# Performance work log

Hardware: AMD Instinct MI355X
Metric: run time of the kernel (lower is better)

Reference implementation:

```python
import jax, jax.numpy as jnp
import numpy as np

B, N, C = 2, 784, 384
D_STATE, D_CONV, EXPAND = 64, 4, 2
D_INNER = EXPAND * C           # 768
DT_RANK = -(-C // 16)          # 24
NB, BS = 4, C // 4             # EinFFT blocks
SCALE = 0.02


def setup_inputs() -> dict:
    key = jax.random.key(0)
    ks = jax.random.split(key, 16)
    rn = lambda k, s, sc=SCALE: jax.random.normal(k, s, jnp.float32) * sc
    A = jnp.tile(jnp.arange(1, D_STATE + 1, dtype=jnp.float32), (D_INNER, 1))
    return {
        'x': jax.random.normal(ks[0], (B, N, C), jnp.float32),
        'H': 28, 'W': 28,
        'ln1_w': jnp.ones((C,), jnp.float32), 'ln1_b': jnp.zeros((C,), jnp.float32),
        'in_proj_w': rn(ks[1], (2 * D_INNER, C)),
        'conv_w': rn(ks[2], (D_INNER, 1, D_CONV), 0.1),
        'conv_b': jnp.zeros((D_INNER,), jnp.float32),
        'x_proj_w': rn(ks[3], (DT_RANK + 2 * D_STATE, D_INNER)),
        'dt_proj_w': rn(ks[4], (D_INNER, DT_RANK), 0.1),
        'dt_proj_b': rn(ks[5], (D_INNER,), 0.1),
        'A_log': jnp.log(A),
        'Dp': jnp.ones((D_INNER,), jnp.float32),
        'out_proj_w': rn(ks[6], (C, D_INNER)),
        'ln2_w': jnp.ones((C,), jnp.float32), 'ln2_b': jnp.zeros((C,), jnp.float32),
        'cw1': rn(ks[7], (2, NB, BS, BS)), 'cb1': rn(ks[8], (2, NB, BS)),
        'cw2': rn(ks[9], (2, NB, BS, BS)), 'cb2': rn(ks[10], (2, NB, BS)),
    }


def _ln(x, w, b, eps=1e-5):
    mu = x.mean(-1, keepdims=True)
    var = ((x - mu) ** 2).mean(-1, keepdims=True)
    return (x - mu) * jax.lax.rsqrt(var + eps) * w + b


def _silu(x):
    return x * jax.nn.sigmoid(x)


def _mamba(x, in_proj_w, conv_w, conv_b, x_proj_w, dt_proj_w, dt_proj_b, A_log, Dp, out_proj_w):
    Bb, L, _ = x.shape
    di, ds = A_log.shape
    dt_rank = dt_proj_w.shape[1]
    xz = x @ in_proj_w.T                       # [B,L,2*di]
    xi, z = jnp.split(xz, 2, axis=-1)
    # causal depthwise conv1d (pad left d_conv-1)
    xc = jax.lax.conv_general_dilated(
        xi.transpose(0, 2, 1), conv_w, (1,), [(conv_w.shape[-1] - 1, 0)],
        feature_group_count=di, dimension_numbers=('NCH', 'OIH', 'NCH'))
    xc = _silu(xc + conv_b[None, :, None]).transpose(0, 2, 1)  # [B,L,di]
    dbl = xc @ x_proj_w.T
    dt, Bs, Cs = jnp.split(dbl, [dt_rank, dt_rank + ds], axis=-1)
    dt = jax.nn.softplus(dt @ dt_proj_w.T + dt_proj_b)          # [B,L,di]
    A = -jnp.exp(A_log)                                          # [di,ds]

    def step(h, inp):
        dt_t, B_t, C_t, u_t = inp                                # [B,di],[B,ds],[B,ds],[B,di]
        dA = jnp.exp(dt_t[:, :, None] * A)                       # [B,di,ds]
        h = h * dA + dt_t[:, :, None] * B_t[:, None, :] * u_t[:, :, None]
        y = jnp.einsum('bds,bs->bd', h, C_t)
        return h, y

    h0 = jnp.zeros((Bb, di, ds), x.dtype)
    xs = (dt.transpose(1, 0, 2), Bs.transpose(1, 0, 2), Cs.transpose(1, 0, 2), xc.transpose(1, 0, 2))
    _, ys = jax.lax.scan(step, h0, xs)                           # [L,B,di]
    y = ys.transpose(1, 0, 2) + xc * Dp
    y = y * _silu(z)
    return y @ out_proj_w.T


def _einfft(x, cw1, cb1, cw2, cb2, lam=0.01):
    Bb, Nn, Cc = x.shape
    nb, bs = cw1.shape[1], cw1.shape[2]
    xf = jnp.fft.fft2(x.reshape(Bb, Nn, nb, bs), axes=(1, 2), norm='ortho')
    mul = lambda t, w: jnp.einsum('...bd,bdk->...bk', t, w)
    r1 = jax.nn.relu(mul(xf.real, cw1[0]) - mul(xf.imag, cw1[1]) + cb1[0])
    i1 = jax.nn.relu(mul(xf.real, cw1[1]) + mul(xf.imag, cw1[0]) + cb1[1])
    r2 = mul(r1, cw2[0]) - mul(i1, cw2[1]) + cb2[0]
    i2 = mul(r1, cw2[1]) + mul(i1, cw2[0]) + cb2[1]
    shrink = lambda v: jnp.sign(v) * jnp.maximum(jnp.abs(v) - lam, 0.0)
    xcplx = shrink(r2) + 1j * shrink(i2)
    out = jnp.fft.ifft2(xcplx, axes=(1, 2), norm='ortho').real.astype(jnp.float32)
    return out.reshape(Bb, Nn, Cc)


def reference(x, H, W, ln1_w, ln1_b, in_proj_w, conv_w, conv_b, x_proj_w,
              dt_proj_w, dt_proj_b, A_log, Dp, out_proj_w, ln2_w, ln2_b,
              cw1, cb1, cw2, cb2):
    x = x + _mamba(_ln(x, ln1_w, ln1_b), in_proj_w, conv_w, conv_b, x_proj_w,
                   dt_proj_w, dt_proj_b, A_log, Dp, out_proj_w)
    x = x + _einfft(_ln(x, ln2_w, ln2_b), cw1, cb1, cw2, cb2)
    return x
```

## Files before the change

kernel.cpp:

```cpp
#include <hip/hip_runtime.h>
#include <math.h>

#define BB 2
#define NN 784
#define CC 384
#define DI 768
#define DS 64
#define DTR 24
#define ROWS (BB*NN)
#define NC 16
#define LC 49

typedef __attribute__((ext_vector_type(8))) short bf16x8;
typedef __attribute__((ext_vector_type(4))) float f32x4;

static __device__ inline short f2bf(float f){
  unsigned u = __float_as_uint(f);
  unsigned r = (u + 0x7fffu + ((u>>16)&1u)) >> 16;
  return (short)r;
}
static __device__ inline float bf2f(short v){
  return __uint_as_float(((unsigned)(unsigned short)v)<<16);
}
static __device__ inline float rdlane(float v, int t){
  return __uint_as_float(__builtin_amdgcn_readlane(__float_as_uint(v), t));
}
template<int CTRL>
static __device__ inline float qp_add(float x){
  int t = __builtin_amdgcn_update_dpp(0, __float_as_int(x), CTRL, 0xf, 0xf, false);
  return x + __int_as_float(t);
}
#define QP_XOR1 0xB1
#define QP_XOR2 0x4E
#define LOG2E 1.44269504088896f

__global__ void k_zero4(float4* __restrict__ p, int n4){
  int i = blockIdx.x*256 + threadIdx.x;
  if (i < n4) p[i] = make_float4(0.f,0.f,0.f,0.f);
}

__global__ void k_ln(const float* __restrict__ x, const float* __restrict__ w,
                     const float* __restrict__ b, short* __restrict__ out, int rows){
  int row = blockIdx.x;
  if (row >= rows) return;
  int lane = threadIdx.x;
  const float* xr = x + (size_t)row*CC;
  float v[6]; float s = 0.f;
#pragma unroll
  for (int i=0;i<6;i++){ v[i] = xr[lane + 64*i]; s += v[i]; }
#pragma unroll
  for (int o=32;o;o>>=1) s += __shfl_xor(s,o);
  float mu = s * (1.f/CC);
  float vs = 0.f;
#pragma unroll
  for (int i=0;i<6;i++){ float d=v[i]-mu; vs += d*d; }
#pragma unroll
  for (int o=32;o;o>>=1) vs += __shfl_xor(vs,o);
  float rstd = rsqrtf(vs*(1.f/CC) + 1e-5f);
  short* orow = out + (size_t)row*CC;
#pragma unroll
  for (int i=0;i<6;i++){ int c = lane+64*i; orow[c] = f2bf((v[i]-mu)*rstd*w[c] + b[c]); }
}

__global__ void k_lnT(const float* __restrict__ x, const float* __restrict__ w,
                      const float* __restrict__ b, short* __restrict__ out){
  int row = blockIdx.x;
  if (row >= ROWS) return;
  int bb = row / NN, n = row % NN;
  int lane = threadIdx.x;
  const float* xr = x + (size_t)row*CC;
  float v[6]; float s = 0.f;
#pragma unroll
  for (int i=0;i<6;i++){ v[i] = xr[lane + 64*i]; s += v[i]; }
#pragma unroll
  for (int o=32;o;o>>=1) s += __shfl_xor(s,o);
  float mu = s * (1.f/CC);
  float vs = 0.f;
#pragma unroll
  for (int i=0;i<6;i++){ float d=v[i]-mu; vs += d*d; }
#pragma unroll
  for (int o=32;o;o>>=1) vs += __shfl_xor(vs,o);
  float rstd = rsqrtf(vs*(1.f/CC) + 1e-5f);
  short* ob = out + (size_t)bb*301056 + n;
#pragma unroll
  for (int i=0;i<6;i++){ int c = lane+64*i; ob[(size_t)c*NN] = f2bf((v[i]-mu)*rstd*w[c] + b[c]); }
}

template<int EPI, int ABF, int BBF, int SPLITK>
__global__ __launch_bounds__(256) void k_mgemm(
    const void* __restrict__ Ap, int lda, long long Azs,
    const void* __restrict__ Bp, int ldb, long long Bzs,
    const float* __restrict__ aux, int ldaux, long long auxzs,
    float* __restrict__ Y, int ldo, long long Ozs,
    int M, int N, int K, float alpha)
{
  __shared__ __align__(16) short As[64*32];
  __shared__ __align__(16) short Bs[64*32];
  int bz = blockIdx.z;
  int z  = bz / SPLITK, ks = bz % SPLITK;
  if (EPI == 1 || EPI == 2 || EPI == 3) aux += (size_t)z*auxzs;
  Y += (size_t)z*Ozs;
  int nk = (K + 31) >> 5;
  int per = (nk + SPLITK - 1) / SPLITK;
  int kbeg = ks*per*32;
  int kend = kbeg + per*32; if (kend > K) kend = K;
  if (kend <= kbeg) return;
  int ntile = (kend - kbeg + 31) >> 5;
  int m0 = blockIdx.y*64, n0 = blockIdx.x*64;
  int t = threadIdx.x;
  int srow = t>>2, skg = t&3;
  int w = t>>6, lane = t&63;
  int wr = (w>>1)*32, wc = (w&1)*32;
  int l15 = lane&15, lh = lane>>4;
  f32x4 acc[2][2] = {};
  int sslot = skg ^ ((srow>>1)&3);
  int gmA = m0 + srow, gnB = n0 + srow;
  int gko = skg*8;

  bf16x8 vA = {}, vB = {};
  float4 fA0, fA1, fB0, fB1;

  auto LOAD = [&](int k0){
    int gk = k0 + gko;
    if (ABF){
      bf16x8 v = {};
      if (gmA < M && gk < K) v = *(const bf16x8*)((const short*)Ap + (size_t)z*Azs + (size_t)gmA*lda + gk);
      vA = v;
    } else {
      fA0 = make_float4(0.f,0.f,0.f,0.f); fA1 = fA0;
      if (gmA < M && gk < K){
        const float* p = (const float*)Ap + (size_t)z*Azs + (size_t)gmA*lda + gk;
        fA0 = *(const float4*)p; fA1 = *(const float4*)(p+4);
      }
    }
    if (BBF){
      bf16x8 v = {};
      if (gnB < N && gk < K) v = *(const bf16x8*)((const short*)Bp + (size_t)z*Bzs + (size_t)gnB*ldb + gk);
      vB = v;
    } else {
      fB0 = make_float4(0.f,0.f,0.f,0.f); fB1 = fB0;
      if (gnB < N && gk < K){
        const float* p = (const float*)Bp + (size_t)z*Bzs + (size_t)gnB*ldb + gk;
        fB0 = *(const float4*)p; fB1 = *(const float4*)(p+4);
      }
    }
  };
  auto STORE = [&](){
    if (ABF) *(bf16x8*)(As + srow*32 + sslot*8) = vA;
    else {
      union { short s[8]; bf16x8 v; } pk;
      pk.s[0]=f2bf(fA0.x); pk.s[1]=f2bf(fA0.y); pk.s[2]=f2bf(fA0.z); pk.s[3]=f2bf(fA0.w);
      pk.s[4]=f2bf(fA1.x); pk.s[5]=f2bf(fA1.y); pk.s[6]=f2bf(fA1.z); pk.s[7]=f2bf(fA1.w);
      *(bf16x8*)(As + srow*32 + sslot*8) = pk.v;
    }
    if (BBF) *(bf16x8*)(Bs + srow*32 + sslot*8) = vB;
    else {
      union { short s[8]; bf16x8 v; } pk;
      pk.s[0]=f2bf(fB0.x); pk.s[1]=f2bf(fB0.y); pk.s[2]=f2bf(fB0.z); pk.s[3]=f2bf(fB0.w);
      pk.s[4]=f2bf(fB1.x); pk.s[5]=f2bf(fB1.y); pk.s[6]=f2bf(fB1.z); pk.s[7]=f2bf(fB1.w);
      *(bf16x8*)(Bs + srow*32 + sslot*8) = pk.v;
    }
  };

  LOAD(kbeg);
  for (int ti=0; ti<ntile; ++ti){
    STORE();
    __syncthreads();
    if (ti+1 < ntile) LOAD(kbeg + (ti+1)*32);
    bf16x8 af[2], bfr[2];
#pragma unroll
    for (int mi=0; mi<2; mi++){
      int row = wr + mi*16 + l15;
      af[mi] = *(const bf16x8*)(As + row*32 + ((lh ^ ((row>>1)&3))<<3));
    }
#pragma unroll
    for (int ni=0; ni<2; ni++){
      int col = wc + ni*16 + l15;
      bfr[ni] = *(const bf16x8*)(Bs + col*32 + ((lh ^ ((col>>1)&3))<<3));
    }
#pragma unroll
    for (int mi=0; mi<2; mi++)
#pragma unroll
      for (int ni=0; ni<2; ni++)
        acc[mi][ni] = __builtin_amdgcn_mfma_f32_16x16x32_bf16(af[mi], bfr[ni], acc[mi][ni], 0, 0, 0);
    __syncthreads();
  }
#pragma unroll
  for (int mi=0; mi<2; mi++){
#pragma unroll
    for (int ni=0; ni<2; ni++){
      int col = n0 + wc + ni*16 + l15;
      if (col >= N) continue;
#pragma unroll
      for (int j=0; j<4; j++){
        int row = m0 + wr + mi*16 + lh*4 + j;
        if (row >= M) continue;
        float v = acc[mi][ni][j];
        if (EPI == 0){ Y[(size_t)row*ldo + col] = v*alpha; }
        else if (EPI == 1){ Y[(size_t)row*ldo + col] = v*alpha + aux[(size_t)row*ldaux + col]; }
        else if (EPI == 2){ v += aux[col]; Y[(size_t)row*ldo + col] = fmaxf(v, 0.f); }
        else if (EPI == 3){ v += aux[col]; Y[(size_t)row*ldo + col] = copysignf(fmaxf(fabsf(v)-0.01f, 0.f), v); }
        else { atomicAdd(&Y[(size_t)row*ldo + col], v*alpha); }
      }
    }
  }
}

#define GBM 64
#define GBN 64
#define GBK 16
__global__ __launch_bounds__(256) void k_gemm(
    const float* __restrict__ X, int lda,
    const float* __restrict__ W,
    const float* __restrict__ bias,
    float* __restrict__ Y,
    int M, int N, int K)
{
  __shared__ float As[GBK][GBM+4];
  __shared__ float Bs[GBK][GBN+4];
  int m0 = blockIdx.y*GBM, n0 = blockIdx.x*GBN;
  int tid = threadIdx.x;
  int ty = tid>>4, tx = tid&15;
  float acc[4][4] = {{0.f}};
  for (int k0=0;k0<K;k0+=GBK){
#pragma unroll
    for (int l=0;l<4;l++){
      int e = tid + 256*l;
      int m = e>>4, kk = e&15;
      int gm = m0+m, gk = k0+kk;
      As[kk][m] = (gm<M && gk<K) ? X[(size_t)gm*lda+gk] : 0.f;
      int gn = n0+m;
      Bs[kk][m] = (gn<N && gk<K) ? W[(size_t)gn*K+gk] : 0.f;
    }
    __syncthreads();
#pragma unroll
    for (int kk=0;kk<GBK;kk++){
      float4 av = *(const float4*)&As[kk][ty*4];
      float4 bv = *(const float4*)&Bs[kk][tx*4];
      float a[4]={av.x,av.y,av.z,av.w}, b[4]={bv.x,bv.y,bv.z,bv.w};
#pragma unroll
      for (int i=0;i<4;i++)
#pragma unroll
        for (int j=0;j<4;j++) acc[i][j] += a[i]*b[j];
    }
    __syncthreads();
  }
#pragma unroll
  for (int i=0;i<4;i++){
    int gm = m0+ty*4+i; if (gm>=M) continue;
#pragma unroll
    for (int j=0;j<4;j++){
      int gn = n0+tx*4+j; if (gn>=N) continue;
      float v = acc[i][j] + bias[gn];
      v = (v>20.f)? v : log1pf(expf(v));
      Y[(size_t)gm*N+gn] = v;
    }
  }
}

__global__ void k_conv(const float* __restrict__ xz, const float* __restrict__ cw,
                       const float* __restrict__ cb, float* __restrict__ xc){
  int idx = blockIdx.x*256 + threadIdx.x;
  if (idx >= ROWS*DI) return;
  int d = idx % DI;
  int r = idx / DI;
  int b = r / NN, l = r % NN;
  float acc = cb[d];
#pragma unroll
  for (int t=0;t<4;t++){
    int ls = l-3+t;
    if (ls>=0) acc += cw[d*4+t] * xz[((size_t)(b*NN+ls))*1536 + d];
  }
  xc[(size_t)r*DI + d] = acc / (1.f + expf(-acc));
}

__global__ __launch_bounds__(256) void k_scan1(
    const float* __restrict__ dbl, const float* __restrict__ dtb,
    const float* __restrict__ xc, const float* __restrict__ A_log,
    short* __restrict__ hpart, float* __restrict__ sdt)
{
  __shared__ float Sb[LC*64];
  int gx = blockIdx.x;
  int bc = gx & 31, dgrp = gx >> 5;
  int b = bc >> 4, c = bc & 15;
  int wv = threadIdx.x >> 6, lane = threadIdx.x & 63;
  int d = dgrp*4 + wv;
  int t0 = c*LC;
  const float* dbr = dbl + ((size_t)(b*NN+t0))*152 + DTR;
  for (int i = threadIdx.x; i < LC*64; i += 256){
    int r = i >> 6, col = i & 63;
    Sb[i] = dbr[(size_t)r*152 + col];
  }
  __syncthreads();
  float A2 = -__expf(A_log[d*DS + lane]) * LOG2E;
  const float* dtp = dtb + ((size_t)(b*NN+t0))*DI + d;
  const float* up  = xc  + ((size_t)(b*NN+t0))*DI + d;
  float dt0v = (lane<LC) ? dtp[(size_t)lane*DI] : 0.f;
  float u0v  = (lane<LC) ? up[(size_t)lane*DI]  : 0.f;
  float du0v = dt0v * u0v;
  float h = 0.f;
  for (int tb=0; tb<LC; tb+=7){
    float e[7], f[7];
#pragma unroll
    for (int j=0;j<7;j++){
      int t = tb+j;
      float dt = rdlane(dt0v, t);
      float du = rdlane(du0v, t);
      e[j] = exp2f(dt*A2);
      f[j] = du*Sb[t*64 + lane];
    }
#pragma unroll
    for (int j=0;j<7;j++) h = h*e[j] + f[j];
  }
  int bd = b*DI + d;
  hpart[((size_t)bd*NC + c)*DS + lane] = f2bf(h);
  float s = dt0v;
#pragma unroll
  for (int o=32;o;o>>=1) s += __shfl_xor(s,o);
  if (lane==0) sdt[bd*NC + c] = s;
}

__global__ __launch_bounds__(256) void k_scan2(
    const float* __restrict__ sdt, const float* __restrict__ A_log,
    short* __restrict__ hpart)
{
  int wid = (blockIdx.x*256 + threadIdx.x) >> 6;
  int lane = threadIdx.x & 63;
  if (wid >= BB*DI) return;
  int d = wid % DI;
  float A = -__expf(A_log[d*DS + lane]);
  short* hp = hpart + (size_t)wid*NC*DS + lane;
  const float* sp = sdt + wid*NC;
  float part[NC], pA[NC];
#pragma unroll
  for (int c=0;c<NC;c++){ part[c] = bf2f(hp[(size_t)c*DS]); pA[c] = __expf(A*sp[c]); }
  float h = 0.f;
#pragma unroll
  for (int c=0;c<NC;c++){
    hp[(size_t)c*DS] = f2bf(h);
    h = h*pA[c] + part[c];
  }
}

__global__ __launch_bounds__(256) void k_scan3(
    const float* __restrict__ dbl, const float* __restrict__ dtb,
    const float* __restrict__ xc, const float* __restrict__ xz,
    const float* __restrict__ A_log, const float* __restrict__ Dp,
    const short* __restrict__ hin, float* __restrict__ y)
{
  __shared__ float S[LC*128];
  __shared__ float red[4][LC*17];
  int gx = blockIdx.x;
  int bc = gx & 31, dgrp = gx >> 5;
  int b = bc >> 4, c = bc & 15;
  int wv = threadIdx.x >> 6, lane = threadIdx.x & 63;
  int d = dgrp*4 + wv;
  int t0 = c*LC;
  const float* dbr = dbl + ((size_t)(b*NN+t0))*152 + DTR;
  for (int i = threadIdx.x; i < LC*128; i += 256){
    int r = i >> 7, col = i & 127;
    int ln = col & 63, which = col >> 6;
    S[r*128 + ln*2 + which] = dbr[(size_t)r*152 + col];
  }
  __syncthreads();
  float A2 = -__expf(A_log[d*DS + lane]) * LOG2E;
  float Dv = Dp[d];
  const float* dtp = dtb + ((size_t)(b*NN+t0))*DI + d;
  const float* up  = xc  + ((size_t)(b*NN+t0))*DI + d;
  const float* zp  = xz  + ((size_t)(b*NN+t0))*1536 + DI + d;
  float* yp = y + ((size_t)(b*NN+t0))*DI + d;
  float dt0v = (lane<LC) ? dtp[(size_t)lane*DI]  : 0.f;
  float u0v  = (lane<LC) ? up[(size_t)lane*DI]   : 0.f;
  float z0v  = (lane<LC) ? zp[(size_t)lane*1536] : 0.f;
  float du0v = dt0v * u0v;
  int bd = b*DI + d;
  float h = bf2f(hin[((size_t)bd*NC + c)*DS + lane]);
  float* rw = red[wv];
  int g = lane>>2;
  bool gl = (lane&3)==0;
  for (int tb=0; tb<LC; tb+=7){
    float e[7], f[7], Cv[7];
#pragma unroll
    for (int j=0;j<7;j++){
      int t = tb+j;
      float2 bcv = *(const float2*)&S[t*128 + lane*2];
      float dt = rdlane(dt0v, t);
      float du = rdlane(du0v, t);
      e[j]  = exp2f(dt*A2);
      f[j]  = du*bcv.x;
      Cv[j] = bcv.y;
    }
#pragma unroll
    for (int j=0;j<7;j++){
      h = h*e[j] + f[j];
      float p = h*Cv[j];
      p = qp_add<QP_XOR1>(p);
      p = qp_add<QP_XOR2>(p);
      if (gl) rw[(tb+j)*17 + g] = p;
    }
  }
  if (lane < LC){
    const float* rr = rw + lane*17;
    float a0 = rr[0]+rr[4]+rr[8] +rr[12];
    float a1 = rr[1]+rr[5]+rr[9] +rr[13];
    float a2 = rr[2]+rr[6]+rr[10]+rr[14];
    float a3 = rr[3]+rr[7]+rr[11]+rr[15];
    float yv = (a0+a1)+(a2+a3) + u0v*Dv;
    float z = z0v;
    yp[(size_t)lane*DI] = yv * (z/(1.f+__expf(-z)));
  }
}

__global__ void k_prep(short* __restrict__ Wcat, short* __restrict__ WT,
                       const float* __restrict__ cw1, const float* __restrict__ cb1,
                       const float* __restrict__ cw2, const float* __restrict__ cb2,
                       short* __restrict__ W1, short* __restrict__ W2,
                       float* __restrict__ b1, float* __restrict__ b2,
                       float4* __restrict__ Ybuf4){
  int idx = blockIdx.x*256+threadIdx.x;
  if (idx < 784*1568){
    int n = idx / 1568, f = idx % 1568;
    int ff = (f<784)? f : f-784;
    int m = (int)(((long long)ff*(long long)n) % 784);
    float ang = 6.283185307179586f * (float)m / 784.f;
    float s, cval; sincosf(ang, &s, &cval);
    WT[(size_t)n*1568 + f] = f2bf((f<784)? cval : -s);
  } else if (idx < 2*784*1568){
    int r = idx - 784*1568;
    int f = r / 784, n = r % 784;
    int ff = (f<784)? f : f-784;
    int m = (int)(((long long)ff*(long long)n) % 784);
    float ang = 6.283185307179586f * (float)m / 784.f;
    float s, cval; sincosf(ang, &s, &cval);
    Wcat[(size_t)f*784 + n] = f2bf((f<784)? cval : -s);
  }
  if (idx < 2*4*192*192){
    int l = idx / (4*192*192);
    int r = idx % (4*192*192);
    int d = r % 192; int j = (r/192) % 192; int bl = r/(192*192);
    int jj = j % 96, dd = d % 96;
    const float* cw = l ? cw2 : cw1;
    const float* w0 = cw + bl*9216;
    const float* w1 = cw + 4*9216 + bl*9216;
    float v;
    if (j < 96) v = (d < 96) ? w0[dd*96+jj] : -w1[dd*96+jj];
    else        v = (d < 96) ? w1[dd*96+jj] :  w0[dd*96+jj];
    (l ? W2 : W1)[r] = f2bf(v);
  }
  if (idx < 2*4*192){
    int l = idx / (4*192);
    int r = idx % (4*192);
    int j = r % 192; int bl = r/192;
    const float* cb = l ? cb2 : cb1;
    (l ? b2 : b1)[r] = (j<96) ? cb[bl*96 + j] : cb[384 + bl*96 + (j-96)];
  }
  if (idx < 301056) Ybuf4[idx] = make_float4(0.f,0.f,0.f,0.f);
}

__global__ void k_cfft4(const float* __restrict__ Ybuf, short* __restrict__ tcat){
  int idx = blockIdx.x*256+threadIdx.x;
  if (idx >= BB*NN*96) return;
  int k = idx % 96; int r = idx / 96;
  int b = r / NN, f = r % NN;
  const float* fre = Ybuf + (size_t)b*602112 + (size_t)f*384;
  const float* fim = fre + 301056;
  float R0=fre[k], R1=fre[96+k], R2=fre[192+k], R3=fre[288+k];
  float I0=fim[k], I1=fim[96+k], I2=fim[192+k], I3=fim[288+k];
  short* tr = tcat + (size_t)r*768;
  tr[k]       = f2bf(R0+R1+R2+R3);  tr[96+k]    = f2bf(I0+I1+I2+I3);
  tr[192+k]   = f2bf(R0+I1-R2-I3);  tr[192+96+k]= f2bf(I0-R1-I2+R3);
  tr[384+k]   = f2bf(R0-R1+R2-R3);  tr[384+96+k]= f2bf(I0-I1+I2-I3);
  tr[576+k]   = f2bf(R0-I1-R2+I3);  tr[576+96+k]= f2bf(I0+R1-I2-R3);
}

__global__ void k_cifft4(const float* __restrict__ t2cat, float* __restrict__ YbufT){
  int idx = blockIdx.x*256+threadIdx.x;
  if (idx >= BB*NN*96) return;
  int f = idx % 784;
  int rest = idx / 784;
  int k = rest % 96;
  int b = rest / 96;
  const float* tr = t2cat + ((size_t)(b*NN+f))*768;
  float R0=tr[k],     I0=tr[96+k];
  float R1=tr[192+k], I1=tr[192+96+k];
  float R2=tr[384+k], I2=tr[384+96+k];
  float R3=tr[576+k], I3=tr[576+96+k];
  float* YT = YbufT + (size_t)b*602112;
  float gr[4], gi[4];
  gr[0]=R0+R1+R2+R3; gi[0]=I0+I1+I2+I3;
  gr[1]=R0-I1-R2+I3; gi[1]=I0+R1-I2-R3;
  gr[2]=R0-R1+R2-R3; gi[2]=I0-I1+I2-I3;
  gr[3]=R0+I1-R2-I3; gi[3]=I0-R1-I2+R3;
#pragma unroll
  for (int n=0;n<4;n++){
    int c = n*96 + k;
    YT[(size_t)c*1568 + f]       = gr[n];
    YT[(size_t)c*1568 + 784 + f] = gi[n];
  }
}

extern "C" void kernel_launch(void* const* d_in, const int* in_sizes, int n_in,
                              void* d_out, int out_size, void* d_ws, size_t ws_size,
                              hipStream_t stream){
  const float* x         = (const float*)d_in[0];
  const float* ln1_w     = (const float*)d_in[3];
  const float* ln1_b     = (const float*)d_in[4];
  const float* in_proj_w = (const float*)d_in[5];
  const float* conv_w    = (const float*)d_in[6];
  const float* conv_b    = (const float*)d_in[7];
  const float* x_proj_w  = (const float*)d_in[8];
  const float* dt_proj_w = (const float*)d_in[9];
  const float* dt_proj_b = (const float*)d_in[10];
  const float* A_log     = (const float*)d_in[11];
  const float* Dp        = (const float*)d_in[12];
  const float* out_proj_w= (const float*)d_in[13];
  const float* ln2_w     = (const float*)d_in[14];
  const float* ln2_b     = (const float*)d_in[15];
  const float* cw1       = (const float*)d_in[16];
  const float* cb1       = (const float*)d_in[17];
  const float* cw2       = (const float*)d_in[18];
  const float* cb2       = (const float*)d_in[19];

  float* ws = (float*)d_ws;
  short* lnb  = (short*)ws;
  float* xz   = ws + 602112;
  float* xc   = ws + 3010560;
  float* dbl  = ws + 4214784;
  float* dtb  = ws + 4453120;
  float* yb   = ws + 5657344;
  float* x1   = ws + 6861568;
  short* hpart= (short*)(ws + 7463680);
  float* sdt  = ws + 8250112;
  short* Wcat = (short*)(ws + 602112);
  short* lnT  = (short*)(ws + 1831424);
  float* Ybuf = ws + 2433536;
  short* WT   = (short*)(ws + 4453120);
  short* tcat = (short*)(ws + 602112);
  float* o1cat= ws + 1806336;
  float* t2cat= ws + 3010560;
  float* YbufT= ws + 602112;
  short* W1c  = (short*)(ws + 7463680);
  short* W2c  = (short*)(ws + 7537408);
  float* b1c  = ws + 7611136;
  float* b2c  = ws + 7611904;

  k_ln<<<ROWS,64,0,stream>>>(x, ln1_w, ln1_b, lnb, ROWS);
  k_mgemm<0,1,0,1><<<dim3(24,25,1),256,0,stream>>>(lnb,384,0, in_proj_w,384,0, nullptr,0,0,
                                                   xz,1536,0, ROWS,1536,384, 1.f);
  k_conv<<<(ROWS*DI+255)/256,256,0,stream>>>(xz,conv_w,conv_b,xc);
  k_zero4<<<(238336/4+255)/256,256,0,stream>>>((float4*)dbl, 238336/4);
  k_mgemm<4,0,0,8><<<dim3(3,25,8),256,0,stream>>>(xc,768,0, x_proj_w,768,0, nullptr,0,0,
                                                  dbl,152,0, ROWS,152,768, 1.f);
  k_gemm<<<dim3(12,25),256,0,stream>>>(dbl,152,dt_proj_w,dt_proj_b,dtb,ROWS,768,24);
  k_scan1<<<32*192,256,0,stream>>>(dbl,dtb,xc,A_log,hpart,sdt);
  k_scan2<<<(BB*DI)/4,256,0,stream>>>(sdt,A_log,hpart);
  k_scan3<<<32*192,256,0,stream>>>(dbl,dtb,xc,xz,A_log,Dp,hpart,yb);
  hipMemcpyAsync(x1, x, (size_t)602112*4, hipMemcpyDeviceToDevice, stream);
  k_mgemm<4,0,0,4><<<dim3(6,25,4),256,0,stream>>>(yb,768,0, out_proj_w,768,0, nullptr,0,0,
                                                  x1,384,0, ROWS,384,768, 1.f);

  k_prep<<<(2*784*1568+255)/256,256,0,stream>>>(Wcat,WT,cw1,cb1,cw2,cb2,W1c,W2c,b1c,b2c,(float4*)Ybuf);
  k_lnT<<<ROWS,64,0,stream>>>(x1, ln2_w, ln2_b, lnT);
  k_mgemm<4,1,1,4><<<dim3(6,25,8),256,0,stream>>>(Wcat,784,0, lnT,784,301056, nullptr,0,0,
                                                  Ybuf,384,602112, 1568,384,784, 1.f/56.f);
  k_cfft4<<<(BB*NN*96+255)/256,256,0,stream>>>(Ybuf,tcat);
  k_mgemm<2,1,1,1><<<dim3(3,25,4),256,0,stream>>>(tcat,768,192, W1c,192,36864, b1c,0,192,
                                                  o1cat,768,192, ROWS,192,192, 1.f);
  k_mgemm<3,0,1,1><<<dim3(3,25,4),256,0,stream>>>(o1cat,768,192, W2c,192,36864, b2c,0,192,
                                                  t2cat,768,192, ROWS,192,192, 1.f);
  k_cifft4<<<(BB*NN*96+255)/256,256,0,stream>>>(t2cat,YbufT);
  hipMemcpyAsync(d_out, x1, (size_t)602112*4, hipMemcpyDeviceToDevice, stream);
  k_mgemm<4,1,0,7><<<dim3(6,13,14),256,0,stream>>>(WT,1568,0, YbufT,1568,602112, nullptr,0,0,
                                                   (float*)d_out,384,301056, 784,384,1568, 1.f/56.f);
}
```

Before: 249.4 us.

## Precompute DFT twiddle table, fuse zeroing into conv, use MFMA for dt_proj

Adds a small kernel that builds a 784-entry cos/sin table, so k_prep reads twiddles from it instead of calling sincosf per element. The separate dbl zeroing kernel is folded into k_conv. The scalar fp32 dt_proj GEMM is replaced by the bf16 MFMA GEMM with a new softplus epilogue. The scan kernels switch from exp2f with a premultiplied log2e to __expf, and compute dt*u in the loop instead of broadcasting a precomputed product. The aim is fewer launches and less transcendental work in the prep stage, at the cost of bf16 rounding in the dt projection and the x-to-x1 copy moving to the front of the stream.

```diff
diff --git a/kernel.cpp b/kernel.cpp
--- a/kernel.cpp
+++ b/kernel.cpp
@@ -32,11 +32,14 @@
 }
 #define QP_XOR1 0xB1
 #define QP_XOR2 0x4E
-#define LOG2E 1.44269504088896f
-
-__global__ void k_zero4(float4* __restrict__ p, int n4){
+
+__global__ void k_tab(float* __restrict__ ct, float* __restrict__ st){
   int i = blockIdx.x*256 + threadIdx.x;
-  if (i < n4) p[i] = make_float4(0.f,0.f,0.f,0.f);
+  if (i < 784){
+    float ang = 6.283185307179586f * (float)i / 784.f;
+    float s, c; sincosf(ang, &s, &c);
+    ct[i] = c; st[i] = s;
+  }
 }
 
 __global__ void k_ln(const float* __restrict__ x, const float* __restrict__ w,
@@ -98,7 +101,7 @@
   __shared__ __align__(16) short Bs[64*32];
   int bz = blockIdx.z;
   int z  = bz / SPLITK, ks = bz % SPLITK;
-  if (EPI == 1 || EPI == 2 || EPI == 3) aux += (size_t)z*auxzs;
+  if (EPI == 1 || EPI == 2 || EPI == 3 || EPI == 5) aux += (size_t)z*auxzs;
   Y += (size_t)z*Ozs;
   int nk = (K + 31) >> 5;
   int per = (nk + SPLITK - 1) / SPLITK;
@@ -200,67 +203,18 @@
         else if (EPI == 1){ Y[(size_t)row*ldo + col] = v*alpha + aux[(size_t)row*ldaux + col]; }
         else if (EPI == 2){ v += aux[col]; Y[(size_t)row*ldo + col] = fmaxf(v, 0.f); }
         else if (EPI == 3){ v += aux[col]; Y[(size_t)row*ldo + col] = copysignf(fmaxf(fabsf(v)-0.01f, 0.f), v); }
+        else if (EPI == 5){ v += aux[col]; Y[(size_t)row*ldo + col] = (v>20.f)? v : log1pf(expf(v)); }
         else { atomicAdd(&Y[(size_t)row*ldo + col], v*alpha); }
       }
     }
   }
 }
 
-#define GBM 64
-#define GBN 64
-#define GBK 16
-__global__ __launch_bounds__(256) void k_gemm(
-    const float* __restrict__ X, int lda,
-    const float* __restrict__ W,
-    const float* __restrict__ bias,
-    float* __restrict__ Y,
-    int M, int N, int K)
-{
-  __shared__ float As[GBK][GBM+4];
-  __shared__ float Bs[GBK][GBN+4];
-  int m0 = blockIdx.y*GBM, n0 = blockIdx.x*GBN;
-  int tid = threadIdx.x;
-  int ty = tid>>4, tx = tid&15;
-  float acc[4][4] = {{0.f}};
-  for (int k0=0;k0<K;k0+=GBK){
-#pragma unroll
-    for (int l=0;l<4;l++){
-      int e = tid + 256*l;
-      int m = e>>4, kk = e&15;
-      int gm = m0+m, gk = k0+kk;
-      As[kk][m] = (gm<M && gk<K) ? X[(size_t)gm*lda+gk] : 0.f;
-      int gn = n0+m;
-      Bs[kk][m] = (gn<N && gk<K) ? W[(size_t)gn*K+gk] : 0.f;
-    }
-    __syncthreads();
-#pragma unroll
-    for (int kk=0;kk<GBK;kk++){
-      float4 av = *(const float4*)&As[kk][ty*4];
-      float4 bv = *(const float4*)&Bs[kk][tx*4];
-      float a[4]={av.x,av.y,av.z,av.w}, b[4]={bv.x,bv.y,bv.z,bv.w};
-#pragma unroll
-      for (int i=0;i<4;i++)
-#pragma unroll
-        for (int j=0;j<4;j++) acc[i][j] += a[i]*b[j];
-    }
-    __syncthreads();
-  }
-#pragma unroll
-  for (int i=0;i<4;i++){
-    int gm = m0+ty*4+i; if (gm>=M) continue;
-#pragma unroll
-    for (int j=0;j<4;j++){
-      int gn = n0+tx*4+j; if (gn>=N) continue;
-      float v = acc[i][j] + bias[gn];
-      v = (v>20.f)? v : log1pf(expf(v));
-      Y[(size_t)gm*N+gn] = v;
-    }
-  }
-}
-
 __global__ void k_conv(const float* __restrict__ xz, const float* __restrict__ cw,
-                       const float* __restrict__ cb, float* __restrict__ xc){
+                       const float* __restrict__ cb, float* __restrict__ xc,
+                       float4* __restrict__ dbl4){
   int idx = blockIdx.x*256 + threadIdx.x;
+  if (idx < 238336/4) dbl4[idx] = make_float4(0.f,0.f,0.f,0.f);
   if (idx >= ROWS*DI) return;
   int d = idx % DI;
   int r = idx / DI;
@@ -292,12 +246,11 @@
     Sb[i] = dbr[(size_t)r*152 + col];
   }
   __syncthreads();
-  float A2 = -__expf(A_log[d*DS + lane]) * LOG2E;
+  float A = -__expf(A_log[d*DS + lane]);
   const float* dtp = dtb + ((size_t)(b*NN+t0))*DI + d;
   const float* up  = xc  + ((size_t)(b*NN+t0))*DI + d;
   float dt0v = (lane<LC) ? dtp[(size_t)lane*DI] : 0.f;
   float u0v  = (lane<LC) ? up[(size_t)lane*DI]  : 0.f;
-  float du0v = dt0v * u0v;
   float h = 0.f;
   for (int tb=0; tb<LC; tb+=7){
     float e[7], f[7];
@@ -305,9 +258,9 @@
     for (int j=0;j<7;j++){
       int t = tb+j;
       float dt = rdlane(dt0v, t);
-      float du = rdlane(du0v, t);
-      e[j] = exp2f(dt*A2);
-      f[j] = du*Sb[t*64 + lane];
+      float u  = rdlane(u0v, t);
+      e[j] = __expf(dt*A);
+      f[j] = (dt*u)*Sb[t*64 + lane];
     }
 #pragma unroll
     for (int j=0;j<7;j++) h = h*e[j] + f[j];
@@ -363,7 +316,7 @@
     S[r*128 + ln*2 + which] = dbr[(size_t)r*152 + col];
   }
   __syncthreads();
-  float A2 = -__expf(A_log[d*DS + lane]) * LOG2E;
+  float A = -__expf(A_log[d*DS + lane]);
   float Dv = Dp[d];
   const float* dtp = dtb + ((size_t)(b*NN+t0))*DI + d;
   const float* up  = xc  + ((size_t)(b*NN+t0))*DI + d;
@@ -372,7 +325,6 @@
   float dt0v = (lane<LC) ? dtp[(size_t)lane*DI]  : 0.f;
   float u0v  = (lane<LC) ? up[(size_t)lane*DI]   : 0.f;
   float z0v  = (lane<LC) ? zp[(size_t)lane*1536] : 0.f;
-  float du0v = dt0v * u0v;
   int bd = b*DI + d;
   float h = bf2f(hin[((size_t)bd*NC + c)*DS + lane]);
   float* rw = red[wv];
@@ -385,9 +337,9 @@
       int t = tb+j;
       float2 bcv = *(const float2*)&S[t*128 + lane*2];
       float dt = rdlane(dt0v, t);
-      float du = rdlane(du0v, t);
-      e[j]  = exp2f(dt*A2);
-      f[j]  = du*bcv.x;
+      float u  = rdlane(u0v, t);
+      e[j]  = __expf(dt*A);
+      f[j]  = (dt*u)*bcv.x;
       Cv[j] = bcv.y;
     }
 #pragma unroll
@@ -412,6 +364,7 @@
 }
 
 __global__ void k_prep(short* __restrict__ Wcat, short* __restrict__ WT,
+                       const float* __restrict__ ct, const float* __restrict__ st,
                        const float* __restrict__ cw1, const float* __restrict__ cb1,
                        const float* __restrict__ cw2, const float* __restrict__ cb2,
                        short* __restrict__ W1, short* __restrict__ W2,
@@ -421,18 +374,14 @@
   if (idx < 784*1568){
     int n = idx / 1568, f = idx % 1568;
     int ff = (f<784)? f : f-784;
-    int m = (int)(((long long)ff*(long long)n) % 784);
-    float ang = 6.283185307179586f * (float)m / 784.f;
-    float s, cval; sincosf(ang, &s, &cval);
-    WT[(size_t)n*1568 + f] = f2bf((f<784)? cval : -s);
+    int m = (ff*n) % 784;
+    WT[(size_t)n*1568 + f] = f2bf((f<784)? ct[m] : -st[m]);
   } else if (idx < 2*784*1568){
     int r = idx - 784*1568;
     int f = r / 784, n = r % 784;
     int ff = (f<784)? f : f-784;
-    int m = (int)(((long long)ff*(long long)n) % 784);
-    float ang = 6.283185307179586f * (float)m / 784.f;
-    float s, cval; sincosf(ang, &s, &cval);
-    Wcat[(size_t)f*784 + n] = f2bf((f<784)? cval : -s);
+    int m = (ff*n) % 784;
+    Wcat[(size_t)f*784 + n] = f2bf((f<784)? ct[m] : -st[m]);
   }
   if (idx < 2*4*192*192){
     int l = idx / (4*192*192);
@@ -531,6 +480,8 @@
   float* x1   = ws + 6861568;
   short* hpart= (short*)(ws + 7463680);
   float* sdt  = ws + 8250112;
+  float* ctab = ws + 8274688;
+  float* stab = ws + 8275472;
   short* Wcat = (short*)(ws + 602112);
   short* lnT  = (short*)(ws + 1831424);
   float* Ybuf = ws + 2433536;
@@ -544,22 +495,24 @@
   float* b1c  = ws + 7611136;
   float* b2c  = ws + 7611904;
 
+  k_tab<<<4,256,0,stream>>>(ctab, stab);
+  hipMemcpyAsync(x1, x, (size_t)602112*4, hipMemcpyDeviceToDevice, stream);
+
   k_ln<<<ROWS,64,0,stream>>>(x, ln1_w, ln1_b, lnb, ROWS);
   k_mgemm<0,1,0,1><<<dim3(24,25,1),256,0,stream>>>(lnb,384,0, in_proj_w,384,0, nullptr,0,0,
                                                    xz,1536,0, ROWS,1536,384, 1.f);
-  k_conv<<<(ROWS*DI+255)/256,256,0,stream>>>(xz,conv_w,conv_b,xc);
-  k_zero4<<<(238336/4+255)/256,256,0,stream>>>((float4*)dbl, 238336/4);
+  k_conv<<<(ROWS*DI+255)/256,256,0,stream>>>(xz,conv_w,conv_b,xc,(float4*)dbl);
   k_mgemm<4,0,0,8><<<dim3(3,25,8),256,0,stream>>>(xc,768,0, x_proj_w,768,0, nullptr,0,0,
                                                   dbl,152,0, ROWS,152,768, 1.f);
-  k_gemm<<<dim3(12,25),256,0,stream>>>(dbl,152,dt_proj_w,dt_proj_b,dtb,ROWS,768,24);
+  k_mgemm<5,0,0,1><<<dim3(12,25,1),256,0,stream>>>(dbl,152,0, dt_proj_w,24,0, dt_proj_b,0,0,
+                                                   dtb,768,0, ROWS,768,24, 1.f);
   k_scan1<<<32*192,256,0,stream>>>(dbl,dtb,xc,A_log,hpart,sdt);
   k_scan2<<<(BB*DI)/4,256,0,stream>>>(sdt,A_log,hpart);
   k_scan3<<<32*192,256,0,stream>>>(dbl,dtb,xc,xz,A_log,Dp,hpart,yb);
-  hipMemcpyAsync(x1, x, (size_t)602112*4, hipMemcpyDeviceToDevice, stream);
   k_mgemm<4,0,0,4><<<dim3(6,25,4),256,0,stream>>>(yb,768,0, out_proj_w,768,0, nullptr,0,0,
                                                   x1,384,0, ROWS,384,768, 1.f);
 
-  k_prep<<<(2*784*1568+255)/256,256,0,stream>>>(Wcat,WT,cw1,cb1,cw2,cb2,W1c,W2c,b1c,b2c,(float4*)Ybuf);
+  k_prep<<<(2*784*1568+255)/256,256,0,stream>>>(Wcat,WT,ctab,stab,cw1,cb1,cw2,cb2,W1c,W2c,b1c,b2c,(float4*)Ybuf);
   k_lnT<<<ROWS,64,0,stream>>>(x1, ln2_w, ln2_b, lnT);
   k_mgemm<4,1,1,4><<<dim3(6,25,8),256,0,stream>>>(Wcat,784,0, lnT,784,301056, nullptr,0,0,
                                                   Ybuf,384,602112, 1568,384,784, 1.f/56.f);
```

After: 236.1 us. -5.4%, faster.
